# Optimization experiments

Hardware: AMD Instinct MI355X
Metric: run time of the kernel (lower is better)

Reference implementation:

```python
import jax, jax.numpy as jnp
import numpy as np

TOPK = 1024
C = 32
FC0 = 256
EPS_BN = 1e-5
EPS_NORM = 1e-12


def setup_inputs() -> dict:
    key = jax.random.key(0)
    ks = jax.random.split(key, 8)
    B, L = 128, 16384
    N = B * L
    x = jax.random.normal(ks[0], (N, C), dtype=jnp.float32)
    length = jnp.full((B,), L, dtype=jnp.int32)
    # conv1d_1: Conv1d(32, 1, 1) -> weight [1, 32, 1] ~ vector [32], bias [1]
    w_att = jax.random.normal(ks[1], (C,), dtype=jnp.float32) * (1.0 / np.sqrt(C))
    b_att = jnp.zeros((1,), dtype=jnp.float32)
    # bn_1: BatchNorm1d(1) (eval mode: use running stats)
    g1 = jnp.ones((1,), dtype=jnp.float32)
    be1 = jnp.zeros((1,), dtype=jnp.float32)
    rm1 = jnp.zeros((1,), dtype=jnp.float32)
    rv1 = jnp.ones((1,), dtype=jnp.float32)
    # fc_1: Linear(TOPK*C, FC0)
    fan_in = TOPK * C
    W_fc = jax.random.normal(ks[2], (FC0, fan_in), dtype=jnp.float32) * (1.0 / np.sqrt(fan_in))
    b_fc = jnp.zeros((FC0,), dtype=jnp.float32)
    # bn_2: BatchNorm1d(FC0) (eval mode)
    g2 = jnp.ones((FC0,), dtype=jnp.float32)
    be2 = jnp.zeros((FC0,), dtype=jnp.float32)
    rm2 = jnp.zeros((FC0,), dtype=jnp.float32)
    rv2 = jnp.ones((FC0,), dtype=jnp.float32)
    return {"x": x, "length": length, "w_att": w_att, "b_att": b_att,
            "g1": g1, "be1": be1, "rm1": rm1, "rv1": rv1,
            "W_fc": W_fc, "b_fc": b_fc,
            "g2": g2, "be2": be2, "rm2": rm2, "rv2": rv2}


def reference(x, length, w_att, b_att, g1, be1, rm1, rv1, W_fc, b_fc, g2, be2, rm2, rv2):
    B = length.shape[0]
    N = x.shape[0]
    L = N // B  # equal-length segments (sum(length) == N)
    # attention score: 1x1 conv over channels + BatchNorm1d(1) (eval)
    att = x @ w_att + b_att[0]                                   # [N]
    att = (att - rm1[0]) * (g1[0] / jnp.sqrt(rv1[0] + EPS_BN)) + be1[0]
    # per-segment descending sort + take top TOPK == top_k per segment
    att_b = att.reshape(B, L)                                    # [B, L]
    x_b = x.reshape(B, L, C)                                     # [B, L, C]
    _, idx = jax.lax.top_k(att_b, TOPK)                          # [B, TOPK]
    ranked = jnp.take_along_axis(x_b, idx[:, :, None], axis=1)   # [B, TOPK, C]
    flat = ranked.reshape(B, TOPK * C)                           # [B, TOPK*C]
    # fc_1 + bn_2 (eval) + L2 row-normalize
    out = flat @ W_fc.T + b_fc                                   # [B, FC0]
    out = (out - rm2) * (g2 / jnp.sqrt(rv2 + EPS_BN)) + be2
    nrm = jnp.maximum(jnp.linalg.norm(out, axis=1, keepdims=True), EPS_NORM)
    return out / nrm
```

## Files before the change

kernel.cpp:

```cpp
#include <hip/hip_runtime.h>
#include <stdint.h>

#define CC 32
#define TOPK 1024
#define FC0 256
#define HL 8192

__device__ __forceinline__ uint64_t cex(uint64_t v, int s, bool up, int t)
{
    uint64_t o = (uint64_t)__shfl_xor((unsigned long long)v, s, 64);
    bool left = ((t & s) == 0);
    uint64_t mn = v < o ? v : o;
    uint64_t mx = v < o ? o : v;
    return (left == up) ? mn : mx;
}

__global__ __launch_bounds__(1024)
void k_seltop(const float* __restrict__ x,
              const float* __restrict__ w_att, const float* __restrict__ b_att,
              uint64_t* __restrict__ cand)
{
    __shared__ float tile[512][CC + 1];
    __shared__ uint32_t kv[HL];
    __shared__ uint64_t cv[2048];
    __shared__ uint32_t hist[257];
    __shared__ uint32_t s_prefix, s_k, s_cnt;
    const int t = threadIdx.x;
    const int b = blockIdx.x;
    const int lane = t & 63;
    const uint32_t halfbase = (uint32_t)(b & 1) * HL;

    if (t == 0) { s_prefix = 0; s_k = TOPK; s_cnt = 0; }

    for (int c = 0; c < 16; ++c) {
        const size_t rowbase = (size_t)b * HL + (size_t)c * 512;
        const float4* xv = (const float4*)(x + rowbase * CC);
        __syncthreads();
        #pragma unroll
        for (int i = 0; i < 4; ++i) {
            int e = i * 1024 + t;
            float4 v = xv[e];
            int r = e >> 3, c4 = (e & 7) * 4;
            tile[r][c4 + 0] = v.x; tile[r][c4 + 1] = v.y;
            tile[r][c4 + 2] = v.z; tile[r][c4 + 3] = v.w;
        }
        __syncthreads();
        if (t < 512) {
            float p[8];
            #pragma unroll
            for (int j = 0; j < 8; ++j) {
                float pj = __fmul_rn(tile[t][j], w_att[j]);
                pj = __fmaf_rn(tile[t][8 + j],  w_att[8 + j],  pj);
                pj = __fmaf_rn(tile[t][16 + j], w_att[16 + j], pj);
                pj = __fmaf_rn(tile[t][24 + j], w_att[24 + j], pj);
                p[j] = pj;
            }
            float q0 = __fadd_rn(p[0], p[1]);
            float q1 = __fadd_rn(p[2], p[3]);
            float q2 = __fadd_rn(p[4], p[5]);
            float q3 = __fadd_rn(p[6], p[7]);
            float dot = __fadd_rn(__fadd_rn(q0, q1), __fadd_rn(q2, q3));
            float v = __fadd_rn(dot, b_att[0]);
            uint32_t bits = __float_as_uint(v);
            kv[c * 512 + t] = (bits & 0x80000000u) ? ~bits : (bits | 0x80000000u);
        }
    }
    __syncthreads();

    #pragma unroll
    for (int round = 0; round < 2; ++round) {
        if (t < 257) hist[t] = 0;
        __syncthreads();
        const uint32_t pref = s_prefix;
        const uint32_t k = s_k;
        for (int i = t; i < HL; i += 1024) {
            uint32_t u = kv[i];
            if (round == 0) atomicAdd(&hist[u >> 24], 1u);
            else if ((u >> 24) == pref) atomicAdd(&hist[(u >> 16) & 255u], 1u);
        }
        __syncthreads();
        if (t < 64) {
            int l = t;
            uint32_t h0 = hist[4*l], h1 = hist[4*l+1], h2 = hist[4*l+2], h3 = hist[4*l+3];
            uint32_t s3 = h3, s2 = h2 + s3, s1 = h1 + s2, s0 = h0 + s1;
            uint32_t tot = s0, run = tot;
            #pragma unroll
            for (int off = 1; off < 64; off <<= 1) {
                int src = l + off < 64 ? l + off : 63;
                uint32_t o = __shfl(run, src, 64);
                if (l + off < 64) run += o;
            }
            uint32_t esuf = run - tot;
            hist[4*l]   = s0 + esuf; hist[4*l+1] = s1 + esuf;
            hist[4*l+2] = s2 + esuf; hist[4*l+3] = s3 + esuf;
        }
        __syncthreads();
        if (t < 256) {
            uint32_t st = hist[t], sn = hist[t + 1];
            if (st >= k && sn < k) {
                s_prefix = (pref << 8) | (uint32_t)t;
                s_k = k - sn;
            }
        }
        __syncthreads();
    }
    const uint32_t T = s_prefix << 16;

    for (int i = t; i < HL; i += 1024) {
        bool q = kv[i] >= T;
        unsigned long long m = __ballot(q);
        uint32_t base = 0;
        if (lane == 0 && m)
            base = atomicAdd(&s_cnt, (uint32_t)__popcll(m));
        base = __shfl(base, 0);
        if (q) {
            uint32_t pos = base + (uint32_t)__popcll(m & ((1ULL << lane) - 1ULL));
            if (pos < 2048)
                cv[pos] = ((uint64_t)kv[i] << 32)
                        | (uint64_t)(uint32_t)(~(halfbase + (uint32_t)i));
        }
    }
    __syncthreads();
    const uint32_t mm = s_cnt < 2048u ? s_cnt : 2048u;
    for (int i = t; i < 2048; i += 1024)
        if ((uint32_t)i >= mm) cv[i] = 0ULL;
    __syncthreads();

    {
        uint64_t r0 = cv[t], r1 = cv[t + 1024];
        #pragma unroll
        for (int size = 2; size <= 64; size <<= 1) {
            bool up = ((t & size) == 0);
            #pragma unroll
            for (int s = size >> 1; s > 0; s >>= 1) {
                r0 = cex(r0, s, up, t);
                r1 = cex(r1, s, up, t);
            }
        }
        cv[t] = r0; cv[t + 1024] = r1;
    }
    #pragma unroll
    for (int size = 128; size <= 2048; size <<= 1) {
        for (int s = size >> 1; s >= 64; s >>= 1) {
            __syncthreads();
            int i = ((t & ~(s - 1)) << 1) | (t & (s - 1));
            int j = i | s;
            uint64_t va = cv[i], vb = cv[j];
            bool up = ((i & size) == 0);
            if (up ? (va > vb) : (va < vb)) { cv[i] = vb; cv[j] = va; }
        }
        __syncthreads();
        {
            uint64_t a0 = cv[t], a1 = cv[t + 1024];
            bool up0, up1;
            if (size <= 512)      { up0 = ((t & size) == 0); up1 = up0; }
            else if (size == 1024){ up0 = true;  up1 = false; }
            else                  { up0 = true;  up1 = true;  }
            #pragma unroll
            for (int s = 32; s > 0; s >>= 1) {
                a0 = cex(a0, s, up0, t);
                a1 = cex(a1, s, up1, t);
            }
            cv[t] = a0; cv[t + 1024] = a1;
        }
        __syncthreads();
    }
    cand[(size_t)b * TOPK + t] = cv[2047 - t];
}

__global__ __launch_bounds__(1024)
void k_merge(const uint64_t* __restrict__ cand, int* __restrict__ idx_out)
{
    __shared__ uint64_t cv[2048];
    const int t = threadIdx.x;
    const int seg = blockIdx.x;
    cv[t]        = cand[(size_t)(seg * 2) * TOPK + t];
    cv[1024 + t] = cand[(size_t)(seg * 2 + 1) * TOPK + (1023 - t)];
    __syncthreads();
    for (int s = 1024; s >= 1; s >>= 1) {
        int i = ((t & ~(s - 1)) << 1) | (t & (s - 1));
        int j = i | s;
        uint64_t va = cv[i], vb = cv[j];
        if (va < vb) { cv[i] = vb; cv[j] = va; }
        __syncthreads();
    }
    idx_out[(size_t)seg * TOPK + t] = (int)(~(uint32_t)cv[t]);
}

#define FT 64
#define KCI 32
#define NKC 128
#define KCHUNK 256

__global__ __launch_bounds__(256)
void k_fc(const float* __restrict__ x, const int* __restrict__ idx,
          const float* __restrict__ W, float* __restrict__ part, int L)
{
    __shared__ float flT[KCI][128];
    __shared__ float wT[KCI][FT];
    const int t = threadIdx.x;
    const int kc = blockIdx.x;
    const int fb = blockIdx.y * FT;
    const int tb = t >> 4, tf = t & 15;
    float acc[8][4];
    #pragma unroll
    for (int i = 0; i < 8; ++i)
        #pragma unroll
        for (int j = 0; j < 4; ++j) acc[i][j] = 0.f;

    const int b_ld = t >> 1, half = t & 1;
    for (int sub = 0; sub < KCHUNK / KCI; ++sub) {
        const int kbase = kc * KCHUNK + sub * KCI;
        const int t_idx = kbase >> 5;
        {
            int row = idx[b_ld * TOPK + t_idx];
            row = row < 0 ? 0 : (row >= L ? L - 1 : row);
            const float* src = x + ((size_t)b_ld * L + row) * CC + half * 16;
            #pragma unroll
            for (int q = 0; q < 4; ++q) {
                float4 v = ((const float4*)src)[q];
                int c0 = half * 16 + q * 4;
                flT[c0 + 0][b_ld] = v.x; flT[c0 + 1][b_ld] = v.y;
                flT[c0 + 2][b_ld] = v.z; flT[c0 + 3][b_ld] = v.w;
            }
        }
        {
            #pragma unroll
            for (int i2 = 0; i2 < 2; ++i2) {
                int e = t + i2 * 256;
                int fl = e >> 3, u = e & 7;
                const float4 v = *(const float4*)(W + (size_t)(fb + fl) * (TOPK * CC) + kbase + u * 4);
                wT[u * 4 + 0][fl] = v.x; wT[u * 4 + 1][fl] = v.y;
                wT[u * 4 + 2][fl] = v.z; wT[u * 4 + 3][fl] = v.w;
            }
        }
        __syncthreads();
        #pragma unroll
        for (int kk = 0; kk < KCI; ++kk) {
            float bb[8], ww[4];
            *(float4*)&bb[0] = *(const float4*)&flT[kk][tb * 8];
            *(float4*)&bb[4] = *(const float4*)&flT[kk][tb * 8 + 4];
            *(float4*)&ww[0] = *(const float4*)&wT[kk][tf * 4];
            #pragma unroll
            for (int i = 0; i < 8; ++i)
                #pragma unroll
                for (int j = 0; j < 4; ++j)
                    acc[i][j] = fmaf(bb[i], ww[j], acc[i][j]);
        }
        __syncthreads();
    }
    float* pbase = part + ((size_t)kc * 128) * 256 + fb + tf * 4;
    #pragma unroll
    for (int i = 0; i < 8; ++i) {
        float* dst = pbase + (size_t)(tb * 8 + i) * 256;
        ((float4*)dst)[0] = make_float4(acc[i][0], acc[i][1], acc[i][2], acc[i][3]);
    }
}

__global__ __launch_bounds__(256)
void k_post(const float* __restrict__ part, const float* __restrict__ b_fc,
            const float* __restrict__ g2, const float* __restrict__ be2,
            const float* __restrict__ rm2, const float* __restrict__ rv2,
            float* __restrict__ out)
{
    __shared__ float red[256];
    const int b = blockIdx.x, f = threadIdx.x;
    float s = 0.f;
    #pragma unroll 8
    for (int kc = 0; kc < NKC; ++kc)
        s += part[((size_t)kc * 128 + b) * 256 + f];
    s += b_fc[f];
    float o = (s - rm2[f]) * (g2[f] / sqrtf(rv2[f] + 1e-5f)) + be2[f];
    red[f] = o * o;
    __syncthreads();
    for (int st = 128; st > 0; st >>= 1) {
        if (f < st) red[f] += red[f + st];
        __syncthreads();
    }
    float nrm = fmaxf(sqrtf(red[0]), 1e-12f);
    out[(size_t)b * 256 + f] = o / nrm;
}

extern "C" void kernel_launch(void* const* d_in, const int* in_sizes, int n_in,
                              void* d_out, int out_size, void* d_ws, size_t ws_size,
                              hipStream_t stream)
{
    const float* x     = (const float*)d_in[0];
    const float* w_att = (const float*)d_in[2];
    const float* b_att = (const float*)d_in[3];
    const float* W_fc  = (const float*)d_in[8];
    const float* b_fc  = (const float*)d_in[9];
    const float* g2    = (const float*)d_in[10];
    const float* be2   = (const float*)d_in[11];
    const float* rm2   = (const float*)d_in[12];
    const float* rv2   = (const float*)d_in[13];

    const int N = in_sizes[0] / CC;
    const int B = in_sizes[1];
    const int L = N / B;

    uint8_t* ws = (uint8_t*)d_ws;
    uint64_t* cand = (uint64_t*)(ws);
    int* idx       = (int*)(ws + (size_t)2 * B * TOPK * 8);
    float* part    = (float*)(ws + (size_t)2 * B * TOPK * 8 + (size_t)B * TOPK * 4);

    k_seltop<<<2 * B, 1024, 0, stream>>>(x, w_att, b_att, cand);
    k_merge<<<B, 1024, 0, stream>>>(cand, idx);
    dim3 g3(NKC, FC0 / FT);
    k_fc<<<g3, 256, 0, stream>>>(x, idx, W_fc, part, L);
    k_post<<<B, 256, 0, stream>>>(part, b_fc, g2, be2, rm2, rv2, (float*)d_out);
}
```

Before: 115.4 us.

## Compute attention scores from registers directly and reorder FC grid dimensions

The score pass in k_seltop no longer stages x through a padded shared-memory tile. Each thread now loads one full 32-float row into registers with float4 loads, keeps the weights in registers, and computes the dot product itself. This removes the tile's LDS traffic, the per-chunk barriers and the idle half of the threads, at the cost of more registers and strided per-thread global loads. Separately, the k_fc grid is transposed so that blocks sharing the same K-chunk are adjacent, which should improve cache reuse of the gathered x rows.

```diff
diff --git a/kernel.cpp b/kernel.cpp
--- a/kernel.cpp
+++ b/kernel.cpp
@@ -20,7 +20,6 @@
               const float* __restrict__ w_att, const float* __restrict__ b_att,
               uint64_t* __restrict__ cand)
 {
-    __shared__ float tile[512][CC + 1];
     __shared__ uint32_t kv[HL];
     __shared__ uint64_t cv[2048];
     __shared__ uint32_t hist[257];
@@ -32,38 +31,35 @@
 
     if (t == 0) { s_prefix = 0; s_k = TOPK; s_cnt = 0; }
 
-    for (int c = 0; c < 16; ++c) {
-        const size_t rowbase = (size_t)b * HL + (size_t)c * 512;
-        const float4* xv = (const float4*)(x + rowbase * CC);
-        __syncthreads();
-        #pragma unroll
-        for (int i = 0; i < 4; ++i) {
-            int e = i * 1024 + t;
-            float4 v = xv[e];
-            int r = e >> 3, c4 = (e & 7) * 4;
-            tile[r][c4 + 0] = v.x; tile[r][c4 + 1] = v.y;
-            tile[r][c4 + 2] = v.z; tile[r][c4 + 3] = v.w;
-        }
-        __syncthreads();
-        if (t < 512) {
-            float p[8];
-            #pragma unroll
-            for (int j = 0; j < 8; ++j) {
-                float pj = __fmul_rn(tile[t][j], w_att[j]);
-                pj = __fmaf_rn(tile[t][8 + j],  w_att[8 + j],  pj);
-                pj = __fmaf_rn(tile[t][16 + j], w_att[16 + j], pj);
-                pj = __fmaf_rn(tile[t][24 + j], w_att[24 + j], pj);
-                p[j] = pj;
-            }
-            float q0 = __fadd_rn(p[0], p[1]);
-            float q1 = __fadd_rn(p[2], p[3]);
-            float q2 = __fadd_rn(p[4], p[5]);
-            float q3 = __fadd_rn(p[6], p[7]);
-            float dot = __fadd_rn(__fadd_rn(q0, q1), __fadd_rn(q2, q3));
-            float v = __fadd_rn(dot, b_att[0]);
-            uint32_t bits = __float_as_uint(v);
-            kv[c * 512 + t] = (bits & 0x80000000u) ? ~bits : (bits | 0x80000000u);
-        }
+    float w[CC];
+    #pragma unroll
+    for (int j = 0; j < CC; ++j) w[j] = w_att[j];
+    const float batt = b_att[0];
+
+    const float* xb = x + (size_t)b * HL * CC;
+    for (int rb = 0; rb < 8; ++rb) {
+        const int row = rb * 1024 + t;
+        const float4* src = (const float4*)(xb + (size_t)row * CC);
+        float xr[CC];
+        #pragma unroll
+        for (int q = 0; q < 8; ++q) *(float4*)&xr[q * 4] = src[q];
+        float p[8];
+        #pragma unroll
+        for (int j = 0; j < 8; ++j) {
+            float pj = __fmul_rn(xr[j], w[j]);
+            pj = __fmaf_rn(xr[8 + j],  w[8 + j],  pj);
+            pj = __fmaf_rn(xr[16 + j], w[16 + j], pj);
+            pj = __fmaf_rn(xr[24 + j], w[24 + j], pj);
+            p[j] = pj;
+        }
+        float q0 = __fadd_rn(p[0], p[1]);
+        float q1 = __fadd_rn(p[2], p[3]);
+        float q2 = __fadd_rn(p[4], p[5]);
+        float q3 = __fadd_rn(p[6], p[7]);
+        float dot = __fadd_rn(__fadd_rn(q0, q1), __fadd_rn(q2, q3));
+        float v = __fadd_rn(dot, batt);
+        uint32_t bits = __float_as_uint(v);
+        kv[row] = (bits & 0x80000000u) ? ~bits : (bits | 0x80000000u);
     }
     __syncthreads();
 
@@ -199,8 +195,8 @@
     __shared__ float flT[KCI][128];
     __shared__ float wT[KCI][FT];
     const int t = threadIdx.x;
-    const int kc = blockIdx.x;
-    const int fb = blockIdx.y * FT;
+    const int kc = blockIdx.y;
+    const int fb = blockIdx.x * FT;
     const int tb = t >> 4, tf = t & 15;
     float acc[8][4];
     #pragma unroll
@@ -306,7 +302,7 @@
 
     k_seltop<<<2 * B, 1024, 0, stream>>>(x, w_att, b_att, cand);
     k_merge<<<B, 1024, 0, stream>>>(cand, idx);
-    dim3 g3(NKC, FC0 / FT);
+    dim3 g3(FC0 / FT, NKC);
     k_fc<<<g3, 256, 0, stream>>>(x, idx, W_fc, part, L);
     k_post<<<B, 256, 0, stream>>>(part, b_fc, g2, be2, rm2, rv2, (float*)d_out);
 }
```

Measured after the change: 132.8 us. 15.1% more time.

## Split each segment's top-k selection into quarters and merge four candidate lists

Applied to the files above, without the earlier changes.

Each segment is now handled by four selection blocks of 4096 rows instead of two blocks of 8192, doubling the grid of k_seltop to 512 blocks. Each block also uses less shared memory. The merge kernel now merges four sorted candidate lists using two bitonic merges plus a final merge, which adds merge work and doubles the candidate workspace. The aim is more parallelism and occupancy in the bandwidth-bound scoring and selection phase, at the cost of more sorting work per block and a heavier merge.

```diff
diff --git a/kernel.cpp b/kernel.cpp
--- a/kernel.cpp
+++ b/kernel.cpp
@@ -4,7 +4,7 @@
 #define CC 32
 #define TOPK 1024
 #define FC0 256
-#define HL 8192
+#define QL 4096
 
 __device__ __forceinline__ uint64_t cex(uint64_t v, int s, bool up, int t)
 {
@@ -20,24 +20,24 @@
               const float* __restrict__ w_att, const float* __restrict__ b_att,
               uint64_t* __restrict__ cand)
 {
-    __shared__ float tile[512][CC + 1];
-    __shared__ uint32_t kv[HL];
+    __shared__ float tile[256][CC + 1];
+    __shared__ uint32_t kv[QL];
     __shared__ uint64_t cv[2048];
     __shared__ uint32_t hist[257];
     __shared__ uint32_t s_prefix, s_k, s_cnt;
     const int t = threadIdx.x;
     const int b = blockIdx.x;
     const int lane = t & 63;
-    const uint32_t halfbase = (uint32_t)(b & 1) * HL;
+    const uint32_t qbase = (uint32_t)(b & 3) * QL;
 
     if (t == 0) { s_prefix = 0; s_k = TOPK; s_cnt = 0; }
 
     for (int c = 0; c < 16; ++c) {
-        const size_t rowbase = (size_t)b * HL + (size_t)c * 512;
+        const size_t rowbase = (size_t)b * QL + (size_t)c * 256;
         const float4* xv = (const float4*)(x + rowbase * CC);
         __syncthreads();
         #pragma unroll
-        for (int i = 0; i < 4; ++i) {
+        for (int i = 0; i < 2; ++i) {
             int e = i * 1024 + t;
             float4 v = xv[e];
             int r = e >> 3, c4 = (e & 7) * 4;
@@ -45,7 +45,7 @@
             tile[r][c4 + 2] = v.z; tile[r][c4 + 3] = v.w;
         }
         __syncthreads();
-        if (t < 512) {
+        if (t < 256) {
             float p[8];
             #pragma unroll
             for (int j = 0; j < 8; ++j) {
@@ -62,7 +62,7 @@
             float dot = __fadd_rn(__fadd_rn(q0, q1), __fadd_rn(q2, q3));
             float v = __fadd_rn(dot, b_att[0]);
             uint32_t bits = __float_as_uint(v);
-            kv[c * 512 + t] = (bits & 0x80000000u) ? ~bits : (bits | 0x80000000u);
+            kv[c * 256 + t] = (bits & 0x80000000u) ? ~bits : (bits | 0x80000000u);
         }
     }
     __syncthreads();
@@ -73,7 +73,7 @@
         __syncthreads();
         const uint32_t pref = s_prefix;
         const uint32_t k = s_k;
-        for (int i = t; i < HL; i += 1024) {
+        for (int i = t; i < QL; i += 1024) {
             uint32_t u = kv[i];
             if (round == 0) atomicAdd(&hist[u >> 24], 1u);
             else if ((u >> 24) == pref) atomicAdd(&hist[(u >> 16) & 255u], 1u);
@@ -106,7 +106,7 @@
     }
     const uint32_t T = s_prefix << 16;
 
-    for (int i = t; i < HL; i += 1024) {
+    for (int i = t; i < QL; i += 1024) {
         bool q = kv[i] >= T;
         unsigned long long m = __ballot(q);
         uint32_t base = 0;
@@ -117,7 +117,7 @@
             uint32_t pos = base + (uint32_t)__popcll(m & ((1ULL << lane) - 1ULL));
             if (pos < 2048)
                 cv[pos] = ((uint64_t)kv[i] << 32)
-                        | (uint64_t)(uint32_t)(~(halfbase + (uint32_t)i));
+                        | (uint64_t)(uint32_t)(~(qbase + (uint32_t)i));
         }
     }
     __syncthreads();
@@ -172,10 +172,36 @@
 void k_merge(const uint64_t* __restrict__ cand, int* __restrict__ idx_out)
 {
     __shared__ uint64_t cv[2048];
+    __shared__ uint64_t tmp[1024];
     const int t = threadIdx.x;
     const int seg = blockIdx.x;
-    cv[t]        = cand[(size_t)(seg * 2) * TOPK + t];
-    cv[1024 + t] = cand[(size_t)(seg * 2 + 1) * TOPK + (1023 - t)];
+    const uint64_t* c0 = cand + (size_t)(seg * 4) * TOPK;
+    cv[t]        = c0[t];
+    cv[1024 + t] = c0[TOPK + (1023 - t)];
+    __syncthreads();
+    for (int s = 1024; s >= 1; s >>= 1) {
+        int i = ((t & ~(s - 1)) << 1) | (t & (s - 1));
+        int j = i | s;
+        uint64_t va = cv[i], vb = cv[j];
+        if (va < vb) { cv[i] = vb; cv[j] = va; }
+        __syncthreads();
+    }
+    tmp[t] = cv[t];
+    __syncthreads();
+    cv[t]        = c0[2 * TOPK + t];
+    cv[1024 + t] = c0[3 * TOPK + (1023 - t)];
+    __syncthreads();
+    for (int s = 1024; s >= 1; s >>= 1) {
+        int i = ((t & ~(s - 1)) << 1) | (t & (s - 1));
+        int j = i | s;
+        uint64_t va = cv[i], vb = cv[j];
+        if (va < vb) { cv[i] = vb; cv[j] = va; }
+        __syncthreads();
+    }
+    uint64_t hi23 = cv[1023 - t];
+    __syncthreads();
+    cv[1024 + t] = hi23;
+    cv[t] = tmp[t];
     __syncthreads();
     for (int s = 1024; s >= 1; s >>= 1) {
         int i = ((t & ~(s - 1)) << 1) | (t & (s - 1));
@@ -301,10 +327,10 @@
 
     uint8_t* ws = (uint8_t*)d_ws;
     uint64_t* cand = (uint64_t*)(ws);
-    int* idx       = (int*)(ws + (size_t)2 * B * TOPK * 8);
-    float* part    = (float*)(ws + (size_t)2 * B * TOPK * 8 + (size_t)B * TOPK * 4);
-
-    k_seltop<<<2 * B, 1024, 0, stream>>>(x, w_att, b_att, cand);
+    int* idx       = (int*)(ws + (size_t)4 * B * TOPK * 8);
+    float* part    = (float*)(ws + (size_t)4 * B * TOPK * 8 + (size_t)B * TOPK * 4);
+
+    k_seltop<<<4 * B, 1024, 0, stream>>>(x, w_att, b_att, cand);
     k_merge<<<B, 1024, 0, stream>>>(cand, idx);
     dim3 g3(NKC, FC0 / FT);
     k_fc<<<g3, 256, 0, stream>>>(x, idx, W_fc, part, L);
```

New measurement: 127.3 us. 1.1x slower.

## Split select kernel into key-select and separate bitonic sort kernels

Applied to the files above, without the earlier changes.

Splits the fused score/radix-select/sort kernel into two kernels. The first writes its unsorted candidates and their count to global workspace, and the second loads them and runs the bitonic sort. This frees 16 KB of LDS in the select kernel, which could allow more resident blocks or waves. In exchange it adds a kernel launch and a global round trip of the candidate buffer.

```diff
diff --git a/kernel.cpp b/kernel.cpp
--- a/kernel.cpp
+++ b/kernel.cpp
@@ -16,13 +16,12 @@
 }
 
 __global__ __launch_bounds__(1024)
-void k_seltop(const float* __restrict__ x,
+void k_keysel(const float* __restrict__ x,
               const float* __restrict__ w_att, const float* __restrict__ b_att,
-              uint64_t* __restrict__ cand)
+              uint64_t* __restrict__ cand_raw, uint32_t* __restrict__ cnt_buf)
 {
     __shared__ float tile[512][CC + 1];
     __shared__ uint32_t kv[HL];
-    __shared__ uint64_t cv[2048];
     __shared__ uint32_t hist[257];
     __shared__ uint32_t s_prefix, s_k, s_cnt;
     const int t = threadIdx.x;
@@ -106,6 +105,7 @@
     }
     const uint32_t T = s_prefix << 16;
 
+    uint64_t* dst = cand_raw + (size_t)b * 2048;
     for (int i = t; i < HL; i += 1024) {
         bool q = kv[i] >= T;
         unsigned long long m = __ballot(q);
@@ -116,16 +116,27 @@
         if (q) {
             uint32_t pos = base + (uint32_t)__popcll(m & ((1ULL << lane) - 1ULL));
             if (pos < 2048)
-                cv[pos] = ((uint64_t)kv[i] << 32)
-                        | (uint64_t)(uint32_t)(~(halfbase + (uint32_t)i));
-        }
-    }
-    __syncthreads();
-    const uint32_t mm = s_cnt < 2048u ? s_cnt : 2048u;
-    for (int i = t; i < 2048; i += 1024)
-        if ((uint32_t)i >= mm) cv[i] = 0ULL;
-    __syncthreads();
-
+                dst[pos] = ((uint64_t)kv[i] << 32)
+                         | (uint64_t)(uint32_t)(~(halfbase + (uint32_t)i));
+        }
+    }
+    __syncthreads();
+    if (t == 0) cnt_buf[b] = s_cnt < 2048u ? s_cnt : 2048u;
+}
+
+__global__ __launch_bounds__(1024)
+void k_sort(const uint64_t* __restrict__ cand_raw,
+            const uint32_t* __restrict__ cnt_buf,
+            uint64_t* __restrict__ cand)
+{
+    __shared__ uint64_t cv[2048];
+    const int t = threadIdx.x;
+    const int b = blockIdx.x;
+    const uint32_t cnt = cnt_buf[b];
+    const uint64_t* src = cand_raw + (size_t)b * 2048;
+    cv[t]        = t < (int)cnt ? src[t] : 0ULL;
+    cv[1024 + t] = 1024 + t < (int)cnt ? src[1024 + t] : 0ULL;
+    __syncthreads();
     {
         uint64_t r0 = cv[t], r1 = cv[t + 1024];
         #pragma unroll
@@ -299,12 +310,21 @@
     const int B = in_sizes[1];
     const int L = N / B;
 
+    const size_t off_cand_raw = 0;
+    const size_t off_cnt      = off_cand_raw + (size_t)2 * B * 2048 * 8;
+    const size_t off_cand     = off_cnt + 4096;
+    const size_t off_idx      = off_cand + (size_t)2 * B * TOPK * 8;
+    const size_t off_part     = off_idx + (size_t)B * TOPK * 4;
+
     uint8_t* ws = (uint8_t*)d_ws;
-    uint64_t* cand = (uint64_t*)(ws);
-    int* idx       = (int*)(ws + (size_t)2 * B * TOPK * 8);
-    float* part    = (float*)(ws + (size_t)2 * B * TOPK * 8 + (size_t)B * TOPK * 4);
-
-    k_seltop<<<2 * B, 1024, 0, stream>>>(x, w_att, b_att, cand);
+    uint64_t* cand_raw = (uint64_t*)(ws + off_cand_raw);
+    uint32_t* cnt_buf  = (uint32_t*)(ws + off_cnt);
+    uint64_t* cand     = (uint64_t*)(ws + off_cand);
+    int* idx           = (int*)(ws + off_idx);
+    float* part        = (float*)(ws + off_part);
+
+    k_keysel<<<2 * B, 1024, 0, stream>>>(x, w_att, b_att, cand_raw, cnt_buf);
+    k_sort<<<2 * B, 1024, 0, stream>>>(cand_raw, cnt_buf, cand);
     k_merge<<<B, 1024, 0, stream>>>(cand, idx);
     dim3 g3(NKC, FC0 / FT);
     k_fc<<<g3, 256, 0, stream>>>(x, idx, W_fc, part, L);
```

After: 117.5 us. About the same (+1.9%).
